# Performance work log

Measured on AMD Instinct MI355X. Metric: run time of the kernel, lower is better.

Reference implementation:

```python
import jax, jax.numpy as jnp
import numpy as np

F_NODE, F_BOND, D, LAYERS = 133, 14, 256, 3
N_NODE, N_BOND, N_NB = 100000, 200000, 600000


def hardswish(x):
    return x * jnp.clip(x + 3.0, 0.0, 6.0) * (1.0 / 6.0)


def setup_inputs() -> dict:
    key = jax.random.key(0)
    ks = jax.random.split(key, 16)

    def xav(k, fan_in, fan_out):
        std = (2.0 / (fan_in + fan_out)) ** 0.5
        return (jax.random.normal(k, (fan_in, fan_out), jnp.float32) * std)

    inp = {
        "node": jax.random.normal(ks[0], (N_NODE, F_NODE), jnp.float32),
        "bond": jax.random.normal(ks[1], (N_BOND, F_BOND), jnp.float32),
        "connect": jax.random.randint(ks[2], (3, N_BOND), 0, N_NODE, jnp.int32),
        "bond_neighbour": jax.random.randint(ks[3], (2, N_NB), 0, N_BOND, jnp.int32),
        # learned parameters, stored as [in, out] (torch Linear transposed)
        "w_node": xav(ks[4], F_NODE, D), "b_node": jnp.zeros((D,), jnp.float32),
        "w_node_final": xav(ks[5], F_NODE + D, D), "b_node_final": jnp.zeros((D,), jnp.float32),
        "w_bond": xav(ks[6], F_NODE + F_BOND, D), "b_bond": jnp.zeros((D,), jnp.float32),
        "w_bond_final": xav(ks[7], F_NODE + F_BOND + D, D), "b_bond_final": jnp.zeros((D,), jnp.float32),
        "w_z": xav(ks[8], F_NODE + F_BOND + D, D), "b_z": jnp.zeros((D,), jnp.float32),
        "w_r": xav(ks[9], F_NODE + F_BOND + D, D), "b_r": jnp.zeros((D,), jnp.float32),
        "u": xav(ks[10], D, D),
        "w_m": xav(ks[11], F_NODE + F_BOND, D), "b_m": jnp.zeros((D,), jnp.float32),
        "w_n": xav(ks[12], F_NODE, D), "b_n": jnp.zeros((D,), jnp.float32),
        "u_n": xav(ks[13], 2 * D, D),
    }
    return inp


def reference(node, bond, connect, bond_neighbour,
              w_node, b_node, w_node_final, b_node_final,
              w_bond, b_bond, w_bond_final, b_bond_final,
              w_z, b_z, w_r, b_r, u, w_m, b_m, w_n, b_n, u_n):
    i_idx, j_idx = connect[0], connect[1]          # [E]; connect[2] (reverse) unused
    ij_idx, ki_idx = bond_neighbour[0], bond_neighbour[1]  # [E_nb]

    init_bond = jnp.concatenate([node[i_idx], bond], axis=-1)  # [E, f_node+f_bond]
    init_node = node                                           # [N, f_node]

    mess_bond = hardswish(init_bond @ w_bond + b_bond)  # [E, D]
    mess_node = hardswish(node @ w_node + b_node)       # [N, D]

    for _ in range(LAYERS):
        mess_ki = mess_bond[ki_idx]                                   # [E_nb, D]
        s_ij = jax.ops.segment_sum(mess_ki, ij_idx, num_segments=N_BOND)
        z_ij = jax.nn.sigmoid(jnp.concatenate([init_bond, s_ij], -1) @ w_z + b_z)
        r_ki = jax.nn.sigmoid(jnp.concatenate([init_bond[ij_idx], mess_ki], -1) @ w_r + b_r)
        r_ij = jax.ops.segment_sum(r_ki * mess_ki, ij_idx, num_segments=N_BOND)
        m_ij = jnp.tanh(init_bond @ w_m + b_m + r_ij @ u)
        mess_bond = (1.0 - z_ij) * s_ij + z_ij * m_ij                 # [E, D]
        aggr_node = jax.ops.segment_sum(mess_bond, j_idx, num_segments=N_NODE)
        mess_node = hardswish(init_node @ w_n + b_n
                              + jnp.concatenate([mess_node, aggr_node], -1) @ u_n)

    mess_bond = hardswish(jnp.concatenate([init_bond, mess_bond], -1) @ w_bond_final + b_bond_final)
    mess_node = hardswish(jnp.concatenate([init_node, mess_node], -1) @ w_node_final + b_node_final)
    # dropout is identity in eval mode
    return mess_node, mess_bond
```

## Files before the change

### kernel.cpp

```cpp
#include <hip/hip_runtime.h>
#include <hip/hip_bf16.h>

#define NN 100000
#define NE 200000
#define NB 600000
#define FN 133
#define FB 14
#define FIB 147
#define DD 256
#define MTS 512
#define NEPAD (196 * 1024)
#define NNPAD (98 * 1024)

typedef __hip_bfloat16 bf16;
typedef __attribute__((ext_vector_type(8))) short short8;
typedef __attribute__((ext_vector_type(4))) float f32x4;

__device__ __forceinline__ float hswish(float x) {
    float c = fminf(fmaxf(x + 3.f, 0.f), 6.f);
    return x * c * (1.f / 6.f);
}
__device__ __forceinline__ float sigmoidf(float x) {
    return 1.f / (1.f + __expf(-x));
}
__device__ __forceinline__ float tanh_fast(float x) {
    return 1.f - 2.f / (1.f + __expf(2.f * x));
}
__device__ __forceinline__ float bf2f(unsigned short u) {
    union { unsigned int i; float f; } c; c.i = (unsigned int)u << 16; return c.f;
}
__device__ __forceinline__ unsigned short f2bf(float v) {
    bf16 b = __float2bfloat16(v);
    unsigned short u; __builtin_memcpy(&u, &b, 2); return u;
}
__device__ __forceinline__ void unp8(short8 v, float* f) {
    #pragma unroll
    for (int j = 0; j < 8; j++) {
        short s = v[j]; unsigned short u; __builtin_memcpy(&u, &s, 2);
        f[j] = bf2f(u);
    }
}
__device__ __forceinline__ uint4 pk8(const float* f) {
    uint4 v;
    v.x = f2bf(f[0]) | ((unsigned)f2bf(f[1]) << 16);
    v.y = f2bf(f[2]) | ((unsigned)f2bf(f[3]) << 16);
    v.z = f2bf(f[4]) | ((unsigned)f2bf(f[5]) << 16);
    v.w = f2bf(f[6]) | ((unsigned)f2bf(f[7]) << 16);
    return v;
}

__global__ __launch_bounds__(256) void fill_kernel(float* __restrict__ p, float v, long n4) {
    long i = (long)blockIdx.x * 256 + threadIdx.x;
    long st = (long)gridDim.x * 256;
    float4 z = {v, v, v, v};
    for (; i < n4; i += st) ((float4*)p)[i] = z;
}

__global__ __launch_bounds__(256) void build_ib_bf(
    const float* __restrict__ node, const float* __restrict__ bond,
    const int* __restrict__ i_idx, bf16* __restrict__ IB)
{
    int t = blockIdx.x * 256 + threadIdx.x;
    int row = t >> 6;
    if (row >= NE) return;
    int lane = t & 63;
    if (lane >= 40) return;
    int src = i_idx[row];
    int c = lane * 4;
    unsigned short us[4];
    #pragma unroll
    for (int j = 0; j < 4; j++) {
        int k = c + j;
        float v = 0.f;
        if (k < FN)       v = node[(size_t)src * FN + k];
        else if (k < FIB) v = bond[(size_t)row * FB + (k - FN)];
        us[j] = f2bf(v);
    }
    ushort4 o = {us[0], us[1], us[2], us[3]};
    *(ushort4*)((unsigned short*)IB + (size_t)row * 160 + c) = o;
}

__global__ __launch_bounds__(256) void zero2_kernel(int* __restrict__ offE, int* __restrict__ offN)
{
    int i = blockIdx.x * 256 + threadIdx.x;
    if (i < NEPAD) offE[i] = 0;
    else if (i < NEPAD + NNPAD) offN[i - NEPAD] = 0;
}

__global__ __launch_bounds__(256) void count2_kernel(
    const int* __restrict__ ij, const int* __restrict__ jidx,
    int* __restrict__ offE, int* __restrict__ offN)
{
    int i = blockIdx.x * 256 + threadIdx.x;
    if (i < NB) atomicAdd(&offE[ij[i]], 1);
    else if (i < NB + NE) atomicAdd(&offN[jidx[i - NB]], 1);
}

__global__ __launch_bounds__(256) void scan_block2(
    int* __restrict__ offE, int* __restrict__ offN,
    int* __restrict__ bsumE, int* __restrict__ bsumN)
{
    __shared__ int lds[256];
    int* data; int* bs; int bb;
    if ((int)blockIdx.x < 196) { data = offE; bs = bsumE; bb = blockIdx.x; }
    else                       { data = offN; bs = bsumN; bb = blockIdx.x - 196; }
    int base = bb * 1024 + threadIdx.x * 4;
    int c0 = data[base], c1 = data[base + 1], c2 = data[base + 2], c3 = data[base + 3];
    int t = c0 + c1 + c2 + c3;
    lds[threadIdx.x] = t;
    __syncthreads();
    int x = t;
    for (int off = 1; off < 256; off <<= 1) {
        int y = (threadIdx.x >= off) ? lds[threadIdx.x - off] : 0;
        __syncthreads();
        x += y; lds[threadIdx.x] = x;
        __syncthreads();
    }
    int excl = x - t;
    data[base] = excl; data[base + 1] = excl + c0;
    data[base + 2] = excl + c0 + c1; data[base + 3] = excl + c0 + c1 + c2;
    if (threadIdx.x == 255) bs[bb] = x;
}

__global__ __launch_bounds__(256) void scan_bsum2(int* __restrict__ bsumE, int* __restrict__ bsumN)
{
    __shared__ int lds[256];
    int* bs = blockIdx.x ? bsumN : bsumE;
    int n = blockIdx.x ? 98 : 196;
    int t = (threadIdx.x < n) ? bs[threadIdx.x] : 0;
    lds[threadIdx.x] = t;
    __syncthreads();
    int x = t;
    for (int off = 1; off < 256; off <<= 1) {
        int y = (threadIdx.x >= off) ? lds[threadIdx.x - off] : 0;
        __syncthreads();
        x += y; lds[threadIdx.x] = x;
        __syncthreads();
    }
    if (threadIdx.x < n) bs[threadIdx.x] = x - t;
}

__global__ __launch_bounds__(256) void scan_add_copy2(
    int* __restrict__ offE, int* __restrict__ offN,
    const int* __restrict__ bsumE, const int* __restrict__ bsumN,
    int* __restrict__ curE, int* __restrict__ curN)
{
    int i = blockIdx.x * 256 + threadIdx.x;
    if (i < NEPAD) {
        int v = offE[i] + bsumE[i >> 10];
        offE[i] = v; curE[i] = v;
    } else if (i < NEPAD + NNPAD) {
        int j = i - NEPAD;
        int v = offN[j] + bsumN[j >> 10];
        offN[j] = v; curN[j] = v;
    }
}

__global__ __launch_bounds__(256) void lists2_kernel(
    const int* __restrict__ ij, const int* __restrict__ ki, const int* __restrict__ jidx,
    int* __restrict__ curE, int* __restrict__ curN,
    int* __restrict__ nbLst, int* __restrict__ agLst)
{
    int i = blockIdx.x * 256 + threadIdx.x;
    if (i < NB) { int p = atomicAdd(&curE[ij[i]], 1); nbLst[p] = ki[i]; }
    else if (i < NB + NE) {
        int e = i - NB;
        int p = atomicAdd(&curN[jidx[e]], 1); agLst[p] = e;
    }
}

__global__ __launch_bounds__(256) void pack_all(
    const float* __restrict__ w_r, const float* __restrict__ w_z,
    const float* __restrict__ w_bond, const float* __restrict__ w_m,
    const float* __restrict__ w_node, const float* __restrict__ w_n,
    const float* __restrict__ u_, const float* __restrict__ u_n,
    const float* __restrict__ w_bf, const float* __restrict__ w_nf,
    bf16* __restrict__ wt)
{
    int idx = blockIdx.x * 256 + threadIdx.x;
    if (idx >= 786432) return;
    float v = 0.f;
    if (idx < 245760) {
        int r = idx / 40960;
        int loc = idx - r * 40960;
        int n = loc / 160, k = loc % 160;
        const float* W = (r == 0) ? w_r : (r == 1) ? w_z : (r == 2) ? w_bond
                       : (r == 3) ? w_m : (r == 4) ? w_node : w_n;
        int K1 = (r < 4) ? FIB : FN;
        if (k < K1) v = W[(size_t)k * DD + n];
    } else if (idx < 442368) {
        int r = (idx - 245760) / 65536;
        int loc = (idx - 245760) - r * 65536;
        int n = loc / 256, k = loc % 256;
        const float* W = (r == 0) ? (w_r + (size_t)FIB * DD)
                       : (r == 1) ? (w_z + (size_t)FIB * DD) : u_;
        v = W[(size_t)k * DD + n];
    } else if (idx < 573440) {
        int loc = idx - 442368;
        int n = loc / 512, k = loc % 512;
        v = u_n[(size_t)k * DD + n];
    } else {
        int r = (idx - 573440) / 106496;
        int loc = (idx - 573440) - r * 106496;
        int n = loc / 416, k = loc % 416;
        const float* W = r ? w_nf : w_bf;
        int K1 = r ? FN : FIB;
        if (k < K1)        v = W[(size_t)k * DD + n];
        else if (k >= 160) v = W[(size_t)(K1 + k - 160) * DD + n];
    }
    wt[idx] = __float2bfloat16(v);
}

__global__ __launch_bounds__(256) void seg_sr_kernel(
    const bf16* __restrict__ MBT, const bf16* __restrict__ PR,
    const int* __restrict__ off, const int* __restrict__ lst,
    bf16* __restrict__ S, bf16* __restrict__ R)
{
    int sid = blockIdx.x * 4 + (threadIdx.x >> 6);
    if (sid >= NE) return;
    int lane = threadIdx.x & 63;
    ushort4 up = *(const ushort4*)((const unsigned short*)PR + (size_t)sid * DD + lane * 4);
    float p0 = bf2f(up.x), p1 = bf2f(up.y), p2 = bf2f(up.z), p3 = bf2f(up.w);
    int b = off[sid], e = off[sid + 1];
    float s0 = 0, s1 = 0, s2 = 0, s3 = 0;
    float r0 = 0, r1 = 0, r2 = 0, r3 = 0;
    for (int t = b; t < e; t++) {
        int src = lst[t];
        const unsigned short* row = (const unsigned short*)MBT + (size_t)src * MTS;
        ushort4 um = *(const ushort4*)(row + lane * 4);
        ushort4 ut = *(const ushort4*)(row + 256 + lane * 4);
        float m0 = bf2f(um.x), m1 = bf2f(um.y), m2 = bf2f(um.z), m3 = bf2f(um.w);
        s0 += m0; s1 += m1; s2 += m2; s3 += m3;
        r0 += sigmoidf(p0 + bf2f(ut.x)) * m0;
        r1 += sigmoidf(p1 + bf2f(ut.y)) * m1;
        r2 += sigmoidf(p2 + bf2f(ut.z)) * m2;
        r3 += sigmoidf(p3 + bf2f(ut.w)) * m3;
    }
    ushort4 os = {f2bf(s0), f2bf(s1), f2bf(s2), f2bf(s3)};
    ushort4 orr = {f2bf(r0), f2bf(r1), f2bf(r2), f2bf(r3)};
    *(ushort4*)((unsigned short*)S + (size_t)sid * DD + lane * 4) = os;
    *(ushort4*)((unsigned short*)R + (size_t)sid * DD + lane * 4) = orr;
}

__global__ __launch_bounds__(512) void blend2(
    const bf16* __restrict__ S, const bf16* __restrict__ R,
    const bf16* __restrict__ WTz2, const bf16* __restrict__ WTu,
    const bf16* __restrict__ PZ, const bf16* __restrict__ PM,
    bf16* __restrict__ MBT)
{
    __shared__ __align__(16) unsigned short As[128 * 72];
    __shared__ __align__(16) unsigned short Bs[128 * 72];
    const int tid = threadIdx.x;
    const int row0 = blockIdx.x * 128, col0 = blockIdx.y * 128;
    const int lane = tid & 63, w = tid >> 6;
    const int wr = w >> 1, wc = w & 1;
    const int fr = lane & 15, ko = (lane >> 4) * 8;

    f32x4 acc1[2][4] = {};
    f32x4 acc2[2][4] = {};

    #pragma unroll
    for (int ph = 0; ph < 2; ph++) {
        const bf16* A = (ph == 0) ? S : R;
        const bf16* W = (ph == 0) ? WTz2 : WTu;
        for (int k0 = 0; k0 < DD; k0 += 64) {
            {
                int mloc = tid >> 2, kq = (tid & 3) * 16;
                int mg = row0 + mloc;
                uint4 va = {0, 0, 0, 0}, va2 = {0, 0, 0, 0};
                if (mg < NE) {
                    va  = *(const uint4*)((const unsigned short*)A + (size_t)mg * DD + k0 + kq);
                    va2 = *(const uint4*)((const unsigned short*)A + (size_t)mg * DD + k0 + kq + 8);
                }
                uint4 vb  = *(const uint4*)((const unsigned short*)W + (size_t)(col0 + mloc) * DD + k0 + kq);
                uint4 vb2 = *(const uint4*)((const unsigned short*)W + (size_t)(col0 + mloc) * DD + k0 + kq + 8);
                *(uint4*)&As[mloc * 72 + kq] = va;
                *(uint4*)&As[mloc * 72 + kq + 8] = va2;
                *(uint4*)&Bs[mloc * 72 + kq] = vb;
                *(uint4*)&Bs[mloc * 72 + kq + 8] = vb2;
            }
            __syncthreads();
            #pragma unroll
            for (int kk = 0; kk < 64; kk += 32) {
                short8 af[2], bf8[4];
                #pragma unroll
                for (int mf = 0; mf < 2; mf++)
                    af[mf] = *(const short8*)&As[(wr * 32 + mf * 16 + fr) * 72 + kk + ko];
                #pragma unroll
                for (int nf = 0; nf < 4; nf++)
                    bf8[nf] = *(const short8*)&Bs[(wc * 64 + nf * 16 + fr) * 72 + kk + ko];
                #pragma unroll
                for (int mf = 0; mf < 2; mf++)
                    #pragma unroll
                    for (int nf = 0; nf < 4; nf++) {
                        if (ph == 0)
                            acc1[mf][nf] = __builtin_amdgcn_mfma_f32_16x16x32_bf16(af[mf], bf8[nf], acc1[mf][nf], 0, 0, 0);
                        else
                            acc2[mf][nf] = __builtin_amdgcn_mfma_f32_16x16x32_bf16(af[mf], bf8[nf], acc2[mf][nf], 0, 0, 0);
                    }
            }
            __syncthreads();
        }
    }

    #pragma unroll
    for (int mf = 0; mf < 2; mf++) {
        #pragma unroll
        for (int i = 0; i < 4; i++) {
            int mloc = wr * 32 + mf * 16 + (lane >> 4) * 4 + i;
            int gm = row0 + mloc;
            if (gm >= NE) continue;
            #pragma unroll
            for (int nf = 0; nf < 4; nf++) {
                int gc = col0 + wc * 64 + nf * 16 + fr;
                size_t idx = (size_t)gm * DD + gc;
                float z  = sigmoidf(acc1[mf][nf][i] + __bfloat162float(PZ[idx]));
                float mm = tanh_fast(acc2[mf][nf][i] + __bfloat162float(PM[idx]));
                float s  = __bfloat162float(S[idx]);
                MBT[(size_t)gm * MTS + gc] = __float2bfloat16((1.f - z) * s + z * mm);
            }
        }
    }
}

__global__ __launch_bounds__(512) void pairk(
    int trblocks,
    const bf16* __restrict__ MBT, const bf16* __restrict__ WTr2,
    const bf16* __restrict__ MN, const int* __restrict__ offN,
    const int* __restrict__ agLst, const bf16* __restrict__ WTnu,
    const bf16* __restrict__ PN, bf16* __restrict__ MNout,
    bf16* __restrict__ MBTw)
{
    __shared__ __align__(16) unsigned short As[128 * 40];
    __shared__ __align__(16) unsigned short Bs[256 * 40];
    const int tid = threadIdx.x, lane = tid & 63, w = tid >> 6;
    const int fr = lane & 15, ko = (lane >> 4) * 8;
    const int mloc = tid >> 2, kq = (tid & 3) * 8;

    if ((int)blockIdx.x < trblocks) {
        const int row0 = blockIdx.x * 128;
        const int wr = w >> 2, wc = w & 3;
        const int mg = row0 + mloc;
        f32x4 acc[4][4] = {};
        for (int k0 = 0; k0 < 256; k0 += 32) {
            uint4 v = {0, 0, 0, 0};
            if (mg < NE)
                v = *(const uint4*)((const unsigned short*)MBT + (size_t)mg * MTS + k0 + kq);
            *(uint4*)&As[mloc * 40 + kq] = v;
            #pragma unroll
            for (int it = 0; it < 2; ++it) {
                int nloc = (tid >> 2) + it * 128;
                *(uint4*)&Bs[nloc * 40 + kq] =
                    *(const uint4*)((const unsigned short*)WTr2 + (size_t)nloc * DD + k0 + kq);
            }
            __syncthreads();
            short8 af[4], bw[4];
            #pragma unroll
            for (int mf = 0; mf < 4; mf++)
                af[mf] = *(const short8*)&As[(wr * 64 + mf * 16 + fr) * 40 + ko];
            #pragma unroll
            for (int nf = 0; nf < 4; nf++)
                bw[nf] = *(const short8*)&Bs[(wc * 64 + nf * 16 + fr) * 40 + ko];
            #pragma unroll
            for (int mf = 0; mf < 4; mf++)
                #pragma unroll
                for (int nf = 0; nf < 4; nf++)
                    acc[mf][nf] = __builtin_amdgcn_mfma_f32_16x16x32_bf16(af[mf], bw[nf], acc[mf][nf], 0, 0, 0);
            __syncthreads();
        }
        #pragma unroll
        for (int mf = 0; mf < 4; mf++)
            #pragma unroll
            for (int i = 0; i < 4; i++) {
                int ml = wr * 64 + mf * 16 + (lane >> 4) * 4 + i;
                int gm = row0 + ml;
                if (gm >= NE) continue;
                #pragma unroll
                for (int nf = 0; nf < 4; nf++) {
                    int gc = wc * 64 + nf * 16 + fr;
                    MBTw[(size_t)gm * MTS + 256 + gc] = __float2bfloat16(acc[mf][nf][i]);
                }
            }
    } else {
        const int bx = blockIdx.x - trblocks;
        const int row0 = bx * 128;
        const int wr = w >> 2, wc = w & 3;
        const int mg = row0 + mloc;
        int eb = 0, ee = 0;
        if (mg < NN) { eb = offN[mg]; ee = offN[mg + 1]; }
        f32x4 acc[4][4] = {};
        for (int k0 = 0; k0 < 512; k0 += 32) {
            const int kg = k0 + kq;
            uint4 v = {0, 0, 0, 0};
            if (mg < NN) {
                if (kg < 256) {
                    v = *(const uint4*)((const unsigned short*)MN + (size_t)mg * DD + kg);
                } else {
                    const int kk = kg - 256;
                    float a[8] = {0, 0, 0, 0, 0, 0, 0, 0};
                    for (int t = eb; t < ee; t++) {
                        int src = agLst[t];
                        float m8[8];
                        unp8(*(const short8*)((const unsigned short*)MBT + (size_t)src * MTS + kk), m8);
                        #pragma unroll
                        for (int j = 0; j < 8; j++) a[j] += m8[j];
                    }
                    v = pk8(a);
                }
            }
            *(uint4*)&As[mloc * 40 + kq] = v;
            #pragma unroll
            for (int it = 0; it < 2; ++it) {
                int nloc = (tid >> 2) + it * 128;
                *(uint4*)&Bs[nloc * 40 + kq] =
                    *(const uint4*)((const unsigned short*)WTnu + (size_t)nloc * 512 + k0 + kq);
            }
            __syncthreads();
            short8 af[4], bw[4];
            #pragma unroll
            for (int mf = 0; mf < 4; mf++)
                af[mf] = *(const short8*)&As[(wr * 64 + mf * 16 + fr) * 40 + ko];
            #pragma unroll
            for (int nf = 0; nf < 4; nf++)
                bw[nf] = *(const short8*)&Bs[(wc * 64 + nf * 16 + fr) * 40 + ko];
            #pragma unroll
            for (int mf = 0; mf < 4; mf++)
                #pragma unroll
                for (int nf = 0; nf < 4; nf++)
                    acc[mf][nf] = __builtin_amdgcn_mfma_f32_16x16x32_bf16(af[mf], bw[nf], acc[mf][nf], 0, 0, 0);
            __syncthreads();
        }
        #pragma unroll
        for (int mf = 0; mf < 4; mf++)
            #pragma unroll
            for (int i = 0; i < 4; i++) {
                int ml = wr * 64 + mf * 16 + (lane >> 4) * 4 + i;
                int gm = row0 + ml;
                if (gm >= NN) continue;
                #pragma unroll
                for (int nf = 0; nf < 4; nf++) {
                    int gc = wc * 64 + nf * 16 + fr;
                    size_t idx = (size_t)gm * DD + gc;
                    MNout[idx] = __float2bfloat16(
                        hswish(acc[mf][nf][i] + __bfloat162float(PN[idx])));
                }
            }
    }
}

template <int BN, int NT, int DUAL, int EPB>
__device__ __forceinline__ void bg_body(
    const void* __restrict__ A1, int a1stride, int a1kw, int a1real, int a1f32,
    const void* __restrict__ A2, int a2stride, int a2kw, int a2real, int a2f32,
    const bf16* __restrict__ WT1, const bf16* __restrict__ WT2, int KT,
    const float* __restrict__ bias1, const float* __restrict__ bias2,
    void* __restrict__ out1, void* __restrict__ out2, int M,
    int row0, int col0, int os1, int os2,
    unsigned short* As, unsigned short* Bs, unsigned short* Bs2)
{
    constexpr int BM = 128;
    constexpr int nWc = BN / 64;
    constexpr int nWr = (NT / 64) / nWc;
    constexpr int MSPAN = BM / nWr;
    constexpr int MFR = MSPAN / 16;
    const int tid = threadIdx.x;
    const int lane = tid & 63, w = tid >> 6;
    const int wr = w / nWc, wc = w % nWc;
    const int fr = lane & 15, ko = (lane >> 4) * 8;

    f32x4 acc[MFR][4] = {};
    f32x4 acc2[DUAL ? MFR : 1][DUAL ? 4 : 1] = {};

    for (int k0 = 0; k0 < KT; k0 += 32) {
        #pragma unroll
        for (int it = 0; it < BM * 4 / NT; ++it) {
            int mloc = (tid >> 2) + it * (NT / 4);
            int mg = row0 + mloc;
            bool mok = (mg < M);
            int kq = (tid & 3) * 8;
            int kg = k0 + kq;
            const void* p; int stride, real, isf; int kk;
            if (kg < a1kw) { p = A1; stride = a1stride; real = a1real; isf = a1f32; kk = kg; }
            else           { p = A2; stride = a2stride; real = a2real; isf = a2f32; kk = kg - a1kw; }
            uint4 v = {0, 0, 0, 0};
            if (mok) {
                if (!isf) {
                    v = *(const uint4*)((const bf16*)p + (size_t)mg * stride + kk);
                } else {
                    const float* fp = (const float*)p + (size_t)mg * stride;
                    unsigned short us[8];
                    #pragma unroll
                    for (int j = 0; j < 8; j++)
                        us[j] = (kk + j < real) ? f2bf(fp[kk + j]) : (unsigned short)0;
                    v.x = us[0] | ((unsigned)us[1] << 16);
                    v.y = us[2] | ((unsigned)us[3] << 16);
                    v.z = us[4] | ((unsigned)us[5] << 16);
                    v.w = us[6] | ((unsigned)us[7] << 16);
                }
            }
            *(uint4*)&As[mloc * 40 + kq] = v;
        }
        #pragma unroll
        for (int it = 0; it < BN * 4 / NT; ++it) {
            int nloc = (tid >> 2) + it * (NT / 4);
            int kq = (tid & 3) * 8;
            *(uint4*)&Bs[nloc * 40 + kq] =
                *(const uint4*)&WT1[(size_t)(col0 + nloc) * KT + k0 + kq];
            if (DUAL)
                *(uint4*)&Bs2[nloc * 40 + kq] =
                    *(const uint4*)&WT2[(size_t)(col0 + nloc) * KT + k0 + kq];
        }
        __syncthreads();
        short8 a1f[MFR], b1f[4], b2f[DUAL ? 4 : 1];
        #pragma unroll
        for (int mf = 0; mf < MFR; mf++)
            a1f[mf] = *(const short8*)&As[(wr * MSPAN + mf * 16 + fr) * 40 + ko];
        #pragma unroll
        for (int nf = 0; nf < 4; nf++) {
            b1f[nf] = *(const short8*)&Bs[(wc * 64 + nf * 16 + fr) * 40 + ko];
            if (DUAL)
                b2f[nf] = *(const short8*)&Bs2[(wc * 64 + nf * 16 + fr) * 40 + ko];
        }
        #pragma unroll
        for (int mf = 0; mf < MFR; mf++)
            #pragma unroll
            for (int nf = 0; nf < 4; nf++) {
                acc[mf][nf] = __builtin_amdgcn_mfma_f32_16x16x32_bf16(a1f[mf], b1f[nf], acc[mf][nf], 0, 0, 0);
                if (DUAL)
                    acc2[mf][nf] = __builtin_amdgcn_mfma_f32_16x16x32_bf16(a1f[mf], b2f[nf], acc2[mf][nf], 0, 0, 0);
            }
        __syncthreads();
    }

    #pragma unroll
    for (int mf = 0; mf < MFR; mf++) {
        #pragma unroll
        for (int i = 0; i < 4; i++) {
            int mloc = wr * MSPAN + mf * 16 + (lane >> 4) * 4 + i;
            int gm = row0 + mloc;
            if (gm >= M) continue;
            #pragma unroll
            for (int nf = 0; nf < 4; nf++) {
                int gc = col0 + wc * 64 + nf * 16 + fr;
                size_t i1 = (size_t)gm * os1 + gc;
                size_t i2 = (size_t)gm * os2 + gc;
                float v = acc[mf][nf][i];
                if (EPB == 0) {
                    if (bias1) v += bias1[gc];
                    ((bf16*)out1)[i1] = __float2bfloat16(v);
                } else if (EPB == 2) {
                    ((bf16*)out1)[i1] = __float2bfloat16(hswish(v + bias1[gc]));
                    ((bf16*)out2)[i2] = __float2bfloat16(acc2[mf][nf][i] + bias2[gc]);
                } else if (EPB == 3) {
                    ((bf16*)out1)[i1] = __float2bfloat16(v + bias1[gc]);
                    ((bf16*)out2)[i2] = __float2bfloat16(acc2[mf][nf][i] + bias2[gc]);
                } else {
                    ((float*)out1)[i1] = hswish(v + bias1[gc]);
                }
            }
        }
    }
}

__device__ __forceinline__ void bg64_body(
    const void* __restrict__ A1, int a1stride, int a1kw, int a1real, int a1f32,
    const void* __restrict__ A2, int a2stride, int a2kw, int a2real, int a2f32,
    const bf16* __restrict__ WT1, int KT, const float* __restrict__ bias1,
    float* __restrict__ out1, int M, int row0,
    unsigned short* As, unsigned short* Bs)
{
    const int tid = threadIdx.x;
    const int lane = tid & 63, w = tid >> 6;
    const int wr = w >> 2, wc = w & 3;
    const int fr = lane & 15, ko = (lane >> 4) * 8;

    f32x4 acc[2][4] = {};

    for (int k0 = 0; k0 < KT; k0 += 32) {
        if (tid < 256) {
            int mloc = tid >> 2, kq = (tid & 3) * 8;
            int mg = row0 + mloc;
            int kg = k0 + kq;
            const void* p; int stride, real, isf; int kk;
            if (kg < a1kw) { p = A1; stride = a1stride; real = a1real; isf = a1f32; kk = kg; }
            else           { p = A2; stride = a2stride; real = a2real; isf = a2f32; kk = kg - a1kw; }
            uint4 v = {0, 0, 0, 0};
            if (mg < M) {
                if (!isf) {
                    v = *(const uint4*)((const bf16*)p + (size_t)mg * stride + kk);
                } else {
                    const float* fp = (const float*)p + (size_t)mg * stride;
                    unsigned short us[8];
                    #pragma unroll
                    for (int j = 0; j < 8; j++)
                        us[j] = (kk + j < real) ? f2bf(fp[kk + j]) : (unsigned short)0;
                    v.x = us[0] | ((unsigned)us[1] << 16);
                    v.y = us[2] | ((unsigned)us[3] << 16);
                    v.z = us[4] | ((unsigned)us[5] << 16);
                    v.w = us[6] | ((unsigned)us[7] << 16);
                }
            }
            *(uint4*)&As[mloc * 40 + kq] = v;
        }
        {
            int kq = (tid & 3) * 8;
            #pragma unroll
            for (int it = 0; it < 2; ++it) {
                int nloc = (tid >> 2) + it * 128;
                *(uint4*)&Bs[nloc * 40 + kq] =
                    *(const uint4*)&WT1[(size_t)nloc * KT + k0 + kq];
            }
        }
        __syncthreads();
        short8 af[2], bw[4];
        #pragma unroll
        for (int mf = 0; mf < 2; mf++)
            af[mf] = *(const short8*)&As[(wr * 32 + mf * 16 + fr) * 40 + ko];
        #pragma unroll
        for (int nf = 0; nf < 4; nf++)
            bw[nf] = *(const short8*)&Bs[(wc * 64 + nf * 16 + fr) * 40 + ko];
        #pragma unroll
        for (int mf = 0; mf < 2; mf++)
            #pragma unroll
            for (int nf = 0; nf < 4; nf++)
                acc[mf][nf] = __builtin_amdgcn_mfma_f32_16x16x32_bf16(af[mf], bw[nf], acc[mf][nf], 0, 0, 0);
        __syncthreads();
    }

    #pragma unroll
    for (int mf = 0; mf < 2; mf++) {
        #pragma unroll
        for (int i = 0; i < 4; i++) {
            int mloc = wr * 32 + mf * 16 + (lane >> 4) * 4 + i;
            int gm = row0 + mloc;
            if (gm >= M) continue;
            #pragma unroll
            for (int nf = 0; nf < 4; nf++) {
                int gc = wc * 64 + nf * 16 + fr;
                out1[(size_t)gm * DD + gc] = hswish(acc[mf][nf][i] + bias1[gc]);
            }
        }
    }
}

__global__ __launch_bounds__(512) void pre_pair1(
    const bf16* __restrict__ IBbf,
    const bf16* __restrict__ WTr, const bf16* __restrict__ WTz1,
    const float* __restrict__ b_r, const float* __restrict__ b_z,
    bf16* __restrict__ PR, bf16* __restrict__ PZ,
    const bf16* __restrict__ WTb, const bf16* __restrict__ WTm1,
    const float* __restrict__ b_bond, const float* __restrict__ b_m,
    bf16* __restrict__ MBT, bf16* __restrict__ PM)
{
    __shared__ __align__(16) unsigned short As[128 * 40];
    __shared__ __align__(16) unsigned short Bs[128 * 40];
    __shared__ __align__(16) unsigned short Bs2[128 * 40];
    int b = blockIdx.x;
    if (b < 3126) {
        int bx = b % 1563, by = b / 1563;
        bg_body<128, 512, 1, 3>(IBbf, 160, 160, 160, 0, nullptr, 0, 0, 0, 0,
            WTr, WTz1, 160, b_r, b_z, PR, PZ, NE, bx * 128, by * 128, DD, DD, As, Bs, Bs2);
    } else {
        int b2 = b - 3126;
        int bx = b2 % 1563, by = b2 / 1563;
        bg_body<128, 512, 1, 2>(IBbf, 160, 160, 160, 0, nullptr, 0, 0, 0, 0,
            WTb, WTm1, 160, b_bond, b_m, MBT, PM, NE, bx * 128, by * 128, MTS, DD, As, Bs, Bs2);
    }
}

__global__ __launch_bounds__(512) void pre_pair2(
    const float* __restrict__ node,
    const bf16* __restrict__ WTn0, const bf16* __restrict__ WTn,
    const float* __restrict__ b_node, const float* __restrict__ b_n,
    bf16* __restrict__ MN, bf16* __restrict__ PN,
    const bf16* __restrict__ MBT, const bf16* __restrict__ WTr2,
    bf16* __restrict__ TRout)
{
    __shared__ __align__(16) unsigned short As[128 * 40];
    __shared__ __align__(16) unsigned short Bs[128 * 40];
    __shared__ __align__(16) unsigned short Bs2[128 * 40];
    int b = blockIdx.x;
    if (b < 1564) {
        int bx = b % 782, by = b / 782;
        bg_body<128, 512, 1, 2>(node, FN, 160, FN, 1, nullptr, 0, 0, 0, 0,
            WTn0, WTn, 160, b_node, b_n, MN, PN, NN, bx * 128, by * 128, DD, DD, As, Bs, Bs2);
    } else {
        int b2 = b - 1564;
        int bx = b2 % 1563, by = b2 / 1563;
        bg_body<128, 512, 0, 0>(MBT, MTS, 256, 256, 0, nullptr, 0, 0, 0, 0,
            WTr2, nullptr, 256, nullptr, nullptr, TRout, nullptr, NE,
            bx * 128, by * 128, MTS, MTS, As, Bs, Bs2);
    }
}

__global__ __launch_bounds__(512) void final_pair64(
    const bf16* __restrict__ IBbf, const bf16* __restrict__ MBT,
    const bf16* __restrict__ WTbf, const float* __restrict__ b_bf,
    float* __restrict__ out_bond,
    const float* __restrict__ node, const bf16* __restrict__ MNf,
    const bf16* __restrict__ WTnf, const float* __restrict__ b_nf,
    float* __restrict__ out_node)
{
    __shared__ __align__(16) unsigned short As[64 * 40];
    __shared__ __align__(16) unsigned short Bs[256 * 40];
    int b = blockIdx.x;
    if (b < 3125) {
        bg64_body(IBbf, 160, 160, 160, 0, MBT, MTS, 256, 256, 0,
                  WTbf, 416, b_bf, out_bond, NE, b * 64, As, Bs);
    } else {
        bg64_body(node, FN, 160, FN, 1, MNf, 256, 256, 256, 0,
                  WTnf, 416, b_nf, out_node, NN, (b - 3125) * 64, As, Bs);
    }
}

extern "C" void kernel_launch(void* const* d_in, const int* in_sizes, int n_in,
                              void* d_out, int out_size, void* d_ws, size_t ws_size,
                              hipStream_t stream)
{
    const float* node  = (const float*)d_in[0];
    const float* bond  = (const float*)d_in[1];
    const int* connect = (const int*)d_in[2];
    const int* bnb     = (const int*)d_in[3];
    const float* w_node       = (const float*)d_in[4];
    const float* b_node       = (const float*)d_in[5];
    const float* w_node_final = (const float*)d_in[6];
    const float* b_node_final = (const float*)d_in[7];
    const float* w_bond       = (const float*)d_in[8];
    const float* b_bond       = (const float*)d_in[9];
    const float* w_bond_final = (const float*)d_in[10];
    const float* b_bond_final = (const float*)d_in[11];
    const float* w_z = (const float*)d_in[12];
    const float* b_z = (const float*)d_in[13];
    const float* w_r = (const float*)d_in[14];
    const float* b_r = (const float*)d_in[15];
    const float* u_  = (const float*)d_in[16];
    const float* w_m = (const float*)d_in[17];
    const float* b_m = (const float*)d_in[18];
    const float* w_n = (const float*)d_in[19];
    const float* b_n = (const float*)d_in[20];
    const float* u_n = (const float*)d_in[21];

    const int* i_idx = connect;
    const int* j_idx = connect + NE;
    const int* ij    = bnb;
    const int* ki    = bnb + NB;

    const size_t EBH = (size_t)NE * DD * 2;
    const size_t B_WT = (size_t)786432 * 2;
    const size_t B_CSR = (size_t)NEPAD * 8 + (size_t)NB * 4
                       + (size_t)NNPAD * 8 + (size_t)NE * 4 + 2048;
    const size_t NEED = 5 * EBH + B_WT + B_CSR;

    float* out_node = (float*)d_out;
    float* out_bond = out_node + (size_t)NN * DD;

    if (ws_size < NEED) {
        fill_kernel<<<2048, 256, 0, stream>>>((float*)d_out, 1e6f, (long)out_size / 4);
        return;
    }

    char* base = (char*)d_ws;
    bf16* PR  = (bf16*)base;                      base += EBH;
    bf16* MBT = (bf16*)base;                      base += 2 * EBH;
    bf16* PZ  = (bf16*)base;                      base += EBH;
    bf16* PM  = (bf16*)base;                      base += EBH;
    char* wt = base;                              base += B_WT;
    int* offE  = (int*)base;                      base += (size_t)NEPAD * 4;
    int* curE  = (int*)base;                      base += (size_t)NEPAD * 4;
    int* nbLst = (int*)base;                      base += (size_t)NB * 4;
    int* offN  = (int*)base;                      base += (size_t)NNPAD * 4;
    int* curN  = (int*)base;                      base += (size_t)NNPAD * 4;
    int* agLst = (int*)base;                      base += (size_t)NE * 4;
    int* bsumE = (int*)base;                      base += 1024;
    int* bsumN = (int*)base;

    bf16* R = (bf16*)out_bond;
    bf16* S = R + (size_t)NE * DD;
    bf16* IBpre = R;
    bf16* IBfin = PZ;
    bf16* MNf = PR;
    bf16* MN = (bf16*)out_node;
    bf16* PN = MN + (size_t)NN * DD;

    bf16* wtb = (bf16*)wt;
    bf16* WTr  = wtb + 0;
    bf16* WTz1 = wtb + 40960;
    bf16* WTb  = wtb + 81920;
    bf16* WTm1 = wtb + 122880;
    bf16* WTn0 = wtb + 163840;
    bf16* WTn  = wtb + 204800;
    bf16* WTr2 = wtb + 245760;
    bf16* WTz2 = wtb + 311296;
    bf16* WTu  = wtb + 376832;
    bf16* WTnu = wtb + 442368;
    bf16* WTbf = wtb + 573440;
    bf16* WTnf = wtb + 679936;

    pack_all<<<3072, 256, 0, stream>>>(w_r, w_z, w_bond, w_m, w_node, w_n,
                                       u_, u_n, w_bond_final, w_node_final, wtb);

    zero2_kernel<<<(NEPAD + NNPAD + 255) / 256, 256, 0, stream>>>(offE, offN);
    count2_kernel<<<(NB + NE + 255) / 256, 256, 0, stream>>>(ij, j_idx, offE, offN);
    scan_block2<<<294, 256, 0, stream>>>(offE, offN, bsumE, bsumN);
    scan_bsum2<<<2, 256, 0, stream>>>(bsumE, bsumN);
    scan_add_copy2<<<(NEPAD + NNPAD + 255) / 256, 256, 0, stream>>>(
        offE, offN, bsumE, bsumN, curE, curN);
    lists2_kernel<<<(NB + NE + 255) / 256, 256, 0, stream>>>(ij, ki, j_idx,
                                                             curE, curN, nbLst, agLst);

    int blkIB = NE * 64 / 256;
    dim3 gB2(1563, 2);

    build_ib_bf<<<blkIB, 256, 0, stream>>>(node, bond, i_idx, IBpre);
    pre_pair1<<<6252, 512, 0, stream>>>(IBpre, WTr, WTz1, b_r, b_z, PR, PZ,
                                        WTb, WTm1, b_bond, b_m, MBT, PM);
    pre_pair2<<<4690, 512, 0, stream>>>(node, WTn0, WTn, b_node, b_n, MN, PN,
                                        MBT, WTr2, MBT + 256);

    for (int l = 0; l < 3; l++) {
        seg_sr_kernel<<<(NE + 3) / 4, 256, 0, stream>>>(MBT, PR, offE, nbLst, S, R);
        blend2<<<gB2, 512, 0, stream>>>(S, R, WTz2, WTu, PZ, PM, MBT);
        int trb = (l < 2) ? 1563 : 0;
        bf16* mnout = (l == 2) ? MNf : MN;
        pairk<<<trb + 782, 512, 0, stream>>>(trb, MBT, WTr2,
                                             MN, offN, agLst, WTnu, PN, mnout, MBT);
    }

    build_ib_bf<<<blkIB, 256, 0, stream>>>(node, bond, i_idx, IBfin);
    final_pair64<<<4688, 512, 0, stream>>>(IBfin, MBT, WTbf, b_bond_final, out_bond,
                                           node, MNf, WTnf, b_node_final, out_node);
}
```

Before: 2.437 ms.

## Fuse neighbour segment-sum gather into the GRU blend GEMM kernel with ping-pong buffers

Merges the segmented gather/reduction that produced S and R with the z/u GEMM-and-blend kernel. Each block gathers 64 rows of neighbour messages, keeps the R and S tiles in shared memory, and runs the MFMA GEMMs directly, so the S/R intermediates no longer make a round trip through global memory. The message buffer is now ping-ponged between two arrays so reads and writes do not alias within a layer. The cost is gathering each neighbour row twice, once for R and once for S, and each block now covers all 256 output columns with 64-row tiles, which changes occupancy and weight reuse.

```diff
diff --git a/kernel.cpp b/kernel.cpp
--- a/kernel.cpp
+++ b/kernel.cpp
@@ -211,96 +211,119 @@
     wt[idx] = __float2bfloat16(v);
 }
 
-__global__ __launch_bounds__(256) void seg_sr_kernel(
-    const bf16* __restrict__ MBT, const bf16* __restrict__ PR,
+__global__ __launch_bounds__(512) void fblend64(
+    const bf16* __restrict__ MBTin, const bf16* __restrict__ PR,
+    const bf16* __restrict__ PZ, const bf16* __restrict__ PM,
     const int* __restrict__ off, const int* __restrict__ lst,
-    bf16* __restrict__ S, bf16* __restrict__ R)
-{
-    int sid = blockIdx.x * 4 + (threadIdx.x >> 6);
-    if (sid >= NE) return;
-    int lane = threadIdx.x & 63;
-    ushort4 up = *(const ushort4*)((const unsigned short*)PR + (size_t)sid * DD + lane * 4);
-    float p0 = bf2f(up.x), p1 = bf2f(up.y), p2 = bf2f(up.z), p3 = bf2f(up.w);
-    int b = off[sid], e = off[sid + 1];
-    float s0 = 0, s1 = 0, s2 = 0, s3 = 0;
-    float r0 = 0, r1 = 0, r2 = 0, r3 = 0;
-    for (int t = b; t < e; t++) {
-        int src = lst[t];
-        const unsigned short* row = (const unsigned short*)MBT + (size_t)src * MTS;
-        ushort4 um = *(const ushort4*)(row + lane * 4);
-        ushort4 ut = *(const ushort4*)(row + 256 + lane * 4);
-        float m0 = bf2f(um.x), m1 = bf2f(um.y), m2 = bf2f(um.z), m3 = bf2f(um.w);
-        s0 += m0; s1 += m1; s2 += m2; s3 += m3;
-        r0 += sigmoidf(p0 + bf2f(ut.x)) * m0;
-        r1 += sigmoidf(p1 + bf2f(ut.y)) * m1;
-        r2 += sigmoidf(p2 + bf2f(ut.z)) * m2;
-        r3 += sigmoidf(p3 + bf2f(ut.w)) * m3;
-    }
-    ushort4 os = {f2bf(s0), f2bf(s1), f2bf(s2), f2bf(s3)};
-    ushort4 orr = {f2bf(r0), f2bf(r1), f2bf(r2), f2bf(r3)};
-    *(ushort4*)((unsigned short*)S + (size_t)sid * DD + lane * 4) = os;
-    *(ushort4*)((unsigned short*)R + (size_t)sid * DD + lane * 4) = orr;
-}
-
-__global__ __launch_bounds__(512) void blend2(
-    const bf16* __restrict__ S, const bf16* __restrict__ R,
     const bf16* __restrict__ WTz2, const bf16* __restrict__ WTu,
-    const bf16* __restrict__ PZ, const bf16* __restrict__ PM,
-    bf16* __restrict__ MBT)
-{
-    __shared__ __align__(16) unsigned short As[128 * 72];
-    __shared__ __align__(16) unsigned short Bs[128 * 72];
+    bf16* __restrict__ MBTout)
+{
+    __shared__ __align__(16) unsigned short Al[64 * 264];
+    __shared__ __align__(16) unsigned short Bs[256 * 40];
     const int tid = threadIdx.x;
-    const int row0 = blockIdx.x * 128, col0 = blockIdx.y * 128;
+    const int row0 = blockIdx.x * 64;
     const int lane = tid & 63, w = tid >> 6;
-    const int wr = w >> 1, wc = w & 1;
+    const int wr = w >> 2, wc = w & 3;
     const int fr = lane & 15, ko = (lane >> 4) * 8;
+    const int sw = tid >> 5, li = tid & 31;
 
     f32x4 acc1[2][4] = {};
     f32x4 acc2[2][4] = {};
 
+    int eb[4], ee[4];
     #pragma unroll
-    for (int ph = 0; ph < 2; ph++) {
-        const bf16* A = (ph == 0) ? S : R;
-        const bf16* W = (ph == 0) ? WTz2 : WTu;
-        for (int k0 = 0; k0 < DD; k0 += 64) {
-            {
-                int mloc = tid >> 2, kq = (tid & 3) * 16;
-                int mg = row0 + mloc;
-                uint4 va = {0, 0, 0, 0}, va2 = {0, 0, 0, 0};
-                if (mg < NE) {
-                    va  = *(const uint4*)((const unsigned short*)A + (size_t)mg * DD + k0 + kq);
-                    va2 = *(const uint4*)((const unsigned short*)A + (size_t)mg * DD + k0 + kq + 8);
-                }
-                uint4 vb  = *(const uint4*)((const unsigned short*)W + (size_t)(col0 + mloc) * DD + k0 + kq);
-                uint4 vb2 = *(const uint4*)((const unsigned short*)W + (size_t)(col0 + mloc) * DD + k0 + kq + 8);
-                *(uint4*)&As[mloc * 72 + kq] = va;
-                *(uint4*)&As[mloc * 72 + kq + 8] = va2;
-                *(uint4*)&Bs[mloc * 72 + kq] = vb;
-                *(uint4*)&Bs[mloc * 72 + kq + 8] = vb2;
-            }
-            __syncthreads();
-            #pragma unroll
-            for (int kk = 0; kk < 64; kk += 32) {
-                short8 af[2], bf8[4];
-                #pragma unroll
-                for (int mf = 0; mf < 2; mf++)
-                    af[mf] = *(const short8*)&As[(wr * 32 + mf * 16 + fr) * 72 + kk + ko];
-                #pragma unroll
-                for (int nf = 0; nf < 4; nf++)
-                    bf8[nf] = *(const short8*)&Bs[(wc * 64 + nf * 16 + fr) * 72 + kk + ko];
-                #pragma unroll
-                for (int mf = 0; mf < 2; mf++)
-                    #pragma unroll
-                    for (int nf = 0; nf < 4; nf++) {
-                        if (ph == 0)
-                            acc1[mf][nf] = __builtin_amdgcn_mfma_f32_16x16x32_bf16(af[mf], bf8[nf], acc1[mf][nf], 0, 0, 0);
-                        else
-                            acc2[mf][nf] = __builtin_amdgcn_mfma_f32_16x16x32_bf16(af[mf], bf8[nf], acc2[mf][nf], 0, 0, 0);
-                    }
-            }
-            __syncthreads();
-        }
+    for (int rr = 0; rr < 4; rr++) {
+        int sid = row0 + sw * 4 + rr;
+        eb[rr] = off[sid]; ee[rr] = off[sid + 1];
+    }
+
+    #pragma unroll
+    for (int rr = 0; rr < 4; rr++) {
+        int r = sw * 4 + rr;
+        int sid = row0 + r;
+        float p[8];
+        unp8(*(const short8*)((const unsigned short*)PR + (size_t)sid * DD + li * 8), p);
+        float a[8] = {0, 0, 0, 0, 0, 0, 0, 0};
+        for (int t = eb[rr]; t < ee[rr]; t++) {
+            int src = lst[t];
+            const unsigned short* row = (const unsigned short*)MBTin + (size_t)src * MTS;
+            float mf8[8], tf[8];
+            unp8(*(const short8*)(row + li * 8), mf8);
+            unp8(*(const short8*)(row + 256 + li * 8), tf);
+            #pragma unroll
+            for (int j = 0; j < 8; j++)
+                a[j] += sigmoidf(p[j] + tf[j]) * mf8[j];
+        }
+        *(uint4*)&Al[r * 264 + li * 8] = pk8(a);
+    }
+    __syncthreads();
+
+    for (int k0 = 0; k0 < DD; k0 += 32) {
+        {
+            int kq = (tid & 3) * 8;
+            #pragma unroll
+            for (int it = 0; it < 2; ++it) {
+                int nloc = (tid >> 2) + it * 128;
+                *(uint4*)&Bs[nloc * 40 + kq] =
+                    *(const uint4*)((const unsigned short*)WTu + (size_t)nloc * DD + k0 + kq);
+            }
+        }
+        __syncthreads();
+        short8 af[2], bw[4];
+        #pragma unroll
+        for (int mf = 0; mf < 2; mf++)
+            af[mf] = *(const short8*)&Al[(wr * 32 + mf * 16 + fr) * 264 + k0 + ko];
+        #pragma unroll
+        for (int nf = 0; nf < 4; nf++)
+            bw[nf] = *(const short8*)&Bs[(wc * 64 + nf * 16 + fr) * 40 + ko];
+        #pragma unroll
+        for (int mf = 0; mf < 2; mf++)
+            #pragma unroll
+            for (int nf = 0; nf < 4; nf++)
+                acc2[mf][nf] = __builtin_amdgcn_mfma_f32_16x16x32_bf16(af[mf], bw[nf], acc2[mf][nf], 0, 0, 0);
+        __syncthreads();
+    }
+
+    #pragma unroll
+    for (int rr = 0; rr < 4; rr++) {
+        int r = sw * 4 + rr;
+        float a[8] = {0, 0, 0, 0, 0, 0, 0, 0};
+        for (int t = eb[rr]; t < ee[rr]; t++) {
+            int src = lst[t];
+            const unsigned short* row = (const unsigned short*)MBTin + (size_t)src * MTS;
+            float mf8[8];
+            unp8(*(const short8*)(row + li * 8), mf8);
+            #pragma unroll
+            for (int j = 0; j < 8; j++) a[j] += mf8[j];
+        }
+        *(uint4*)&Al[r * 264 + li * 8] = pk8(a);
+    }
+    __syncthreads();
+
+    for (int k0 = 0; k0 < DD; k0 += 32) {
+        {
+            int kq = (tid & 3) * 8;
+            #pragma unroll
+            for (int it = 0; it < 2; ++it) {
+                int nloc = (tid >> 2) + it * 128;
+                *(uint4*)&Bs[nloc * 40 + kq] =
+                    *(const uint4*)((const unsigned short*)WTz2 + (size_t)nloc * DD + k0 + kq);
+            }
+        }
+        __syncthreads();
+        short8 af[2], bw[4];
+        #pragma unroll
+        for (int mf = 0; mf < 2; mf++)
+            af[mf] = *(const short8*)&Al[(wr * 32 + mf * 16 + fr) * 264 + k0 + ko];
+        #pragma unroll
+        for (int nf = 0; nf < 4; nf++)
+            bw[nf] = *(const short8*)&Bs[(wc * 64 + nf * 16 + fr) * 40 + ko];
+        #pragma unroll
+        for (int mf = 0; mf < 2; mf++)
+            #pragma unroll
+            for (int nf = 0; nf < 4; nf++)
+                acc1[mf][nf] = __builtin_amdgcn_mfma_f32_16x16x32_bf16(af[mf], bw[nf], acc1[mf][nf], 0, 0, 0);
+        __syncthreads();
     }
 
     #pragma unroll
@@ -309,15 +332,14 @@
         for (int i = 0; i < 4; i++) {
             int mloc = wr * 32 + mf * 16 + (lane >> 4) * 4 + i;
             int gm = row0 + mloc;
-            if (gm >= NE) continue;
             #pragma unroll
             for (int nf = 0; nf < 4; nf++) {
-                int gc = col0 + wc * 64 + nf * 16 + fr;
+                int gc = wc * 64 + nf * 16 + fr;
                 size_t idx = (size_t)gm * DD + gc;
                 float z  = sigmoidf(acc1[mf][nf][i] + __bfloat162float(PZ[idx]));
                 float mm = tanh_fast(acc2[mf][nf][i] + __bfloat162float(PM[idx]));
-                float s  = __bfloat162float(S[idx]);
-                MBT[(size_t)gm * MTS + gc] = __float2bfloat16((1.f - z) * s + z * mm);
+                float s  = bf2f(Al[mloc * 264 + gc]);
+                MBTout[(size_t)gm * MTS + gc] = __float2bfloat16((1.f - z) * s + z * mm);
             }
         }
     }
@@ -760,10 +782,10 @@
     }
 
     char* base = (char*)d_ws;
-    bf16* PR  = (bf16*)base;                      base += EBH;
-    bf16* MBT = (bf16*)base;                      base += 2 * EBH;
-    bf16* PZ  = (bf16*)base;                      base += EBH;
-    bf16* PM  = (bf16*)base;                      base += EBH;
+    bf16* PR   = (bf16*)base;                     base += EBH;
+    bf16* MBTa = (bf16*)base;                     base += 2 * EBH;
+    bf16* PZ   = (bf16*)base;                     base += EBH;
+    bf16* PM   = (bf16*)base;                     base += EBH;
     char* wt = base;                              base += B_WT;
     int* offE  = (int*)base;                      base += (size_t)NEPAD * 4;
     int* curE  = (int*)base;                      base += (size_t)NEPAD * 4;
@@ -774,9 +796,8 @@
     int* bsumE = (int*)base;                      base += 1024;
     int* bsumN = (int*)base;
 
-    bf16* R = (bf16*)out_bond;
-    bf16* S = R + (size_t)NE * DD;
-    bf16* IBpre = R;
+    bf16* MBTb = (bf16*)out_bond;
+    bf16* IBpre = MBTa;
     bf16* IBfin = PZ;
     bf16* MNf = PR;
     bf16* MN = (bf16*)out_node;
@@ -809,24 +830,26 @@
                                                              curE, curN, nbLst, agLst);
 
     int blkIB = NE * 64 / 256;
-    dim3 gB2(1563, 2);
 
     build_ib_bf<<<blkIB, 256, 0, stream>>>(node, bond, i_idx, IBpre);
     pre_pair1<<<6252, 512, 0, stream>>>(IBpre, WTr, WTz1, b_r, b_z, PR, PZ,
-                                        WTb, WTm1, b_bond, b_m, MBT, PM);
+                                        WTb, WTm1, b_bond, b_m, MBTb, PM);
     pre_pair2<<<4690, 512, 0, stream>>>(node, WTn0, WTn, b_node, b_n, MN, PN,
-                                        MBT, WTr2, MBT + 256);
-
+                                        MBTb, WTr2, MBTb + 256);
+
+    bf16* MBr = MBTb;
+    bf16* MBw = MBTa;
     for (int l = 0; l < 3; l++) {
-        seg_sr_kernel<<<(NE + 3) / 4, 256, 0, stream>>>(MBT, PR, offE, nbLst, S, R);
-        blend2<<<gB2, 512, 0, stream>>>(S, R, WTz2, WTu, PZ, PM, MBT);
+        fblend64<<<3125, 512, 0, stream>>>(MBr, PR, PZ, PM, offE, nbLst,
+                                           WTz2, WTu, MBw);
         int trb = (l < 2) ? 1563 : 0;
         bf16* mnout = (l == 2) ? MNf : MN;
-        pairk<<<trb + 782, 512, 0, stream>>>(trb, MBT, WTr2,
-                                             MN, offN, agLst, WTnu, PN, mnout, MBT);
+        pairk<<<trb + 782, 512, 0, stream>>>(trb, MBw, WTr2,
+                                             MN, offN, agLst, WTnu, PN, mnout, MBw);
+        bf16* t = MBr; MBr = MBw; MBw = t;
     }
 
     build_ib_bf<<<blkIB, 256, 0, stream>>>(node, bond, i_idx, IBfin);
-    final_pair64<<<4688, 512, 0, stream>>>(IBfin, MBT, WTbf, b_bond_final, out_bond,
+    final_pair64<<<4688, 512, 0, stream>>>(IBfin, MBTa, WTbf, b_bond_final, out_bond,
                                            node, MNf, WTnf, b_node_final, out_node);
 }
```

After: 3.165 ms. 29.8% more time.
